# Kernel tuning notes

Hardware: AMD Instinct MI355X
Metric: run time of the kernel (lower is better)

## Reference

```python
import jax, jax.numpy as jnp
import numpy as np

B, L, D, K, V = 128, 50, 64, 1024, 100000


def setup_inputs() -> dict:
    key = jax.random.key(0)
    ks = jax.random.split(key, 10)
    s = 0.05
    return {
        "history_item_ids": jax.random.randint(ks[0], (B, L), 0, V, dtype=jnp.int32),
        "history_item_masks": jax.random.randint(ks[1], (B, L), 0, 2, dtype=jnp.int32),
        "embedding_table": jax.random.normal(ks[2], (V, D), jnp.float32) * s,
        "code_book": jax.random.normal(ks[3], (K, D), jnp.float32) * 0.1,
        "Wq": jax.random.normal(ks[4], (D, D), jnp.float32) * s,
        "bq": jnp.zeros((D,), jnp.float32),
        "Wk": jax.random.normal(ks[5], (D, D), jnp.float32) * s,
        "bk": jnp.zeros((D,), jnp.float32),
        "Wv": jax.random.normal(ks[6], (D, D), jnp.float32) * s,
        "bv": jnp.zeros((D,), jnp.float32),
        "W_enc": jax.random.normal(ks[7], (2 * D, D), jnp.float32) * s,
        "b_enc": jnp.zeros((D,), jnp.float32),
    }


def reference(history_item_ids, history_item_masks, embedding_table, code_book,
              Wq, bq, Wk, bk, Wv, bv, W_enc, b_enc):
    # mask out padded history positions
    mask = (history_item_masks >= 1).astype(jnp.float32)          # [B, L]
    h = embedding_table[history_item_ids] * mask[..., None]       # [B, L, D]

    # self_attn: attention over ALL B*L flattened tokens (cross-batch, as original)
    flat = h.reshape(-1, D)                                       # [B*L, D]
    q = flat @ Wq + bq
    k = flat @ Wk + bk
    v = flat @ Wv + bv
    scores = (q @ k.T) / jnp.sqrt(jnp.float32(D))                 # [B*L, B*L]
    h = (jax.nn.softmax(scores, axis=-1) @ v).reshape(B, L, D)

    denom = mask.sum(axis=1, keepdims=True)                       # [B, 1]
    hist_mean = h.sum(axis=1) / (denom + 1e-9)                    # [B, D]

    # get_quantized: pairwise sq distances + argmin + codebook lookup
    f = h.reshape(-1, D)                                          # [B*L, D]
    d2 = (jnp.sum(f * f, axis=1, keepdims=True)
          + jnp.sum(code_book * code_book, axis=1)
          - 2.0 * f @ code_book.T)                                # [B*L, K]
    idx = jnp.argmin(d2, axis=1)                                  # [B*L]
    vq = code_book[idx].reshape(B, L, D)                          # one_hot @ code_book == gather
    vq_mean = vq.sum(axis=1) / denom                              # [B, D]

    x = jnp.concatenate([vq_mean, hist_mean], axis=-1)            # [B, 2D]
    return x @ W_enc + b_enc                                      # [B, D]
```

## Files before the change

kernel.cpp:

```cpp
#include <hip/hip_runtime.h>

typedef __attribute__((ext_vector_type(8))) short bf16x8_t;
typedef __attribute__((ext_vector_type(4))) float f32x4_t;

#define B_   128
#define L_   50
#define D_   64
#define N_   6400
#define KC   1024
#define STRD 72

static __device__ __forceinline__ unsigned short f2b(float x) {
    union { float f; unsigned int u; } c; c.f = x;
    return (unsigned short)((c.u + 0x7FFFu + ((c.u >> 16) & 1u)) >> 16);
}

__global__ __launch_bounds__(256) void k_qkv(
    const int* __restrict__ ids, const int* __restrict__ masks,
    const float* __restrict__ emb,
    const float* __restrict__ Wq, const float* __restrict__ bq,
    const float* __restrict__ Wk, const float* __restrict__ bk,
    const float* __restrict__ Wv, const float* __restrict__ bv,
    const float* __restrict__ cbf,
    unsigned short* __restrict__ q, unsigned short* __restrict__ k,
    unsigned short* __restrict__ vt,
    float* __restrict__ cn, unsigned short* __restrict__ cbb,
    float4* __restrict__ zbase)
{
    const int tid = threadIdx.x;
    if (blockIdx.x >= 404) {
        const float4 z = make_float4(0.f, 0.f, 0.f, 0.f);
        for (int i = (blockIdx.x - 404) * 256 + tid; i < 108096; i += 26 * 256)
            zbase[i] = z;
        return;
    }
    if (blockIdx.x >= 400) {
        const int c = (blockIdx.x - 400) * 256 + tid;
        float s = 0.f;
        #pragma unroll
        for (int d4 = 0; d4 < 16; ++d4) {
            float4 x = ((const float4*)cbf)[c * 16 + d4];
            s = fmaf(x.x, x.x, s); s = fmaf(x.y, x.y, s);
            s = fmaf(x.z, x.z, s); s = fmaf(x.w, x.w, s);
            ushort4 u;
            u.x = f2b(x.x); u.y = f2b(x.y); u.z = f2b(x.z); u.w = f2b(x.w);
            *(ushort4*)&cbb[c * 64 + d4 * 4] = u;
        }
        cn[c] = s;
        return;
    }

    __shared__ float Ws[3 * 64 * 64];
    __shared__ float hs[16][64];
    const int n0  = blockIdx.x * 16;

    {
        const float4* wq4 = (const float4*)Wq;
        const float4* wk4 = (const float4*)Wk;
        const float4* wv4 = (const float4*)Wv;
        float4* ws4 = (float4*)Ws;
        #pragma unroll
        for (int i = 0; i < 4; ++i) ws4[i*256 + tid]        = wq4[i*256 + tid];
        #pragma unroll
        for (int i = 0; i < 4; ++i) ws4[1024 + i*256 + tid] = wk4[i*256 + tid];
        #pragma unroll
        for (int i = 0; i < 4; ++i) ws4[2048 + i*256 + tid] = wv4[i*256 + tid];
    }
    {
        const int t  = tid >> 4, c4 = tid & 15;
        const int n  = n0 + t;
        const int id = ids[n];
        const float m = (masks[n] >= 1) ? 1.0f : 0.0f;
        float4 e = ((const float4*)emb)[id * 16 + c4];
        ((float4*)&hs[t][0])[c4] = make_float4(e.x*m, e.y*m, e.z*m, e.w*m);
    }
    __syncthreads();

    const int j  = tid & 63;
    const int tg = tid >> 6;
    const float bqj = bq[j], bkj = bk[j], bvj = bv[j];
    #pragma unroll
    for (int p = 0; p < 4; ++p) {
        const int t = p * 4 + tg;
        float aq = bqj, ak = bkj, av = bvj;
        #pragma unroll 8
        for (int d = 0; d < 64; ++d) {
            const float hd = hs[t][d];
            aq = fmaf(hd, Ws[d*64 + j],        aq);
            ak = fmaf(hd, Ws[4096 + d*64 + j], ak);
            av = fmaf(hd, Ws[8192 + d*64 + j], av);
        }
        const int n = n0 + t;
        q[n*64 + j]   = f2b(aq);
        k[n*64 + j]   = f2b(ak);
        vt[j*N_ + n]  = f2b(av);
    }
}

__global__ __launch_bounds__(256, 4) void k_attn(
    const unsigned short* __restrict__ qg, const unsigned short* __restrict__ kg,
    const unsigned short* __restrict__ vtg,
    float* __restrict__ facc, float* __restrict__ lacc)
{
    __shared__ unsigned short Qs[32 * STRD];
    __shared__ unsigned short Ks[64 * STRD];
    __shared__ unsigned short Vts[64 * STRD];
    __shared__ unsigned short Ps[32 * STRD];
    __shared__ float Of[32 * 66];
    __shared__ float lred[2][32];

    const int tid  = threadIdx.x;
    const int qt   = blockIdx.x >> 2;
    const int sp   = blockIdx.x & 3;
    const int q0   = qt * 32;
    const int kvb  = sp * 1600;
    const int lane = tid & 63;
    const int w    = tid >> 6;
    const int m    = w & 1;
    const int s    = w >> 1;
    const int lr   = lane & 15;
    const int lg   = lane >> 4;

    {
        const int row = tid >> 3, ch = tid & 7;
        uint4 t = *(const uint4*)&qg[(q0 + row) * 64 + ch * 8];
        *(uint4*)&Qs[row * STRD + ch * 8] = t;
    }
    __syncthreads();
    const bf16x8_t qa0 = *(const bf16x8_t*)&Qs[(m*16 + lr) * STRD +  0 + lg*8];
    const bf16x8_t qa1 = *(const bf16x8_t*)&Qs[(m*16 + lr) * STRD + 32 + lg*8];

    f32x4_t o0 = {0.f,0.f,0.f,0.f}, o1 = {0.f,0.f,0.f,0.f};
    f32x4_t o2 = {0.f,0.f,0.f,0.f}, o3 = {0.f,0.f,0.f,0.f};
    float ls0 = 0.f, ls1 = 0.f, ls2 = 0.f, ls3 = 0.f;
    const float scale = 0.125f;

    for (int st = 0; st < 25; ++st) {
        __syncthreads();
        const int j0 = kvb + st * 64;
        {
            const int row = tid >> 3, ch = tid & 7;
            uint4 a = *(const uint4*)&kg [(j0 + row)      * 64 + ch*8];
            uint4 b = *(const uint4*)&kg [(j0 + row + 32) * 64 + ch*8];
            uint4 c = *(const uint4*)&vtg[ row       * N_ + j0 + ch*8];
            uint4 d = *(const uint4*)&vtg[(row + 32) * N_ + j0 + ch*8];
            *(uint4*)&Ks [ row      * STRD + ch*8] = a;
            *(uint4*)&Ks [(row+32)  * STRD + ch*8] = b;
            *(uint4*)&Vts[ row      * STRD + ch*8] = c;
            *(uint4*)&Vts[(row+32)  * STRD + ch*8] = d;
        }
        __syncthreads();

        #pragma unroll
        for (int t = 0; t < 2; ++t) {
            const int kcol = s*32 + t*16 + lr;
            bf16x8_t kb0 = *(const bf16x8_t*)&Ks[kcol * STRD +  0 + lg*8];
            bf16x8_t kb1 = *(const bf16x8_t*)&Ks[kcol * STRD + 32 + lg*8];
            f32x4_t acc = {0.f,0.f,0.f,0.f};
            acc = __builtin_amdgcn_mfma_f32_16x16x32_bf16(qa0, kb0, acc, 0, 0, 0);
            acc = __builtin_amdgcn_mfma_f32_16x16x32_bf16(qa1, kb1, acc, 0, 0, 0);
            const float p0 = __expf(acc[0] * scale);
            const float p1 = __expf(acc[1] * scale);
            const float p2 = __expf(acc[2] * scale);
            const float p3 = __expf(acc[3] * scale);
            ls0 += p0; ls1 += p1; ls2 += p2; ls3 += p3;
            const int rb = (m*16 + lg*4) * STRD + kcol;
            Ps[rb           ] = f2b(p0);
            Ps[rb +   STRD  ] = f2b(p1);
            Ps[rb + 2*STRD  ] = f2b(p2);
            Ps[rb + 3*STRD  ] = f2b(p3);
        }

        const bf16x8_t pa = *(const bf16x8_t*)&Ps[(m*16 + lr) * STRD + s*32 + lg*8];
        {
            bf16x8_t vb;
            vb = *(const bf16x8_t*)&Vts[( 0 + lr) * STRD + s*32 + lg*8];
            o0 = __builtin_amdgcn_mfma_f32_16x16x32_bf16(pa, vb, o0, 0, 0, 0);
            vb = *(const bf16x8_t*)&Vts[(16 + lr) * STRD + s*32 + lg*8];
            o1 = __builtin_amdgcn_mfma_f32_16x16x32_bf16(pa, vb, o1, 0, 0, 0);
            vb = *(const bf16x8_t*)&Vts[(32 + lr) * STRD + s*32 + lg*8];
            o2 = __builtin_amdgcn_mfma_f32_16x16x32_bf16(pa, vb, o2, 0, 0, 0);
            vb = *(const bf16x8_t*)&Vts[(48 + lr) * STRD + s*32 + lg*8];
            o3 = __builtin_amdgcn_mfma_f32_16x16x32_bf16(pa, vb, o3, 0, 0, 0);
        }
    }

    #pragma unroll
    for (int off = 1; off <= 8; off <<= 1) {
        ls0 += __shfl_xor(ls0, off);
        ls1 += __shfl_xor(ls1, off);
        ls2 += __shfl_xor(ls2, off);
        ls3 += __shfl_xor(ls3, off);
    }
    if (lr == 0) {
        const int rb = m*16 + lg*4;
        lred[s][rb    ] = ls0;
        lred[s][rb + 1] = ls1;
        lred[s][rb + 2] = ls2;
        lred[s][rb + 3] = ls3;
    }

    if (s == 0) {
        #pragma unroll
        for (int r = 0; r < 4; ++r) {
            const int row = m*16 + lg*4 + r;
            Of[row*66 +  0 + lr] = o0[r];
            Of[row*66 + 16 + lr] = o1[r];
            Of[row*66 + 32 + lr] = o2[r];
            Of[row*66 + 48 + lr] = o3[r];
        }
    }
    __syncthreads();
    if (s == 1) {
        #pragma unroll
        for (int r = 0; r < 4; ++r) {
            const int row = m*16 + lg*4 + r;
            float* dst = &facc[(q0 + row) * 64];
            atomicAdd(&dst[ 0 + lr], Of[row*66 +  0 + lr] + o0[r]);
            atomicAdd(&dst[16 + lr], Of[row*66 + 16 + lr] + o1[r]);
            atomicAdd(&dst[32 + lr], Of[row*66 + 32 + lr] + o2[r]);
            atomicAdd(&dst[48 + lr], Of[row*66 + 48 + lr] + o3[r]);
        }
    }
    if (tid < 32) atomicAdd(&lacc[q0 + tid], lred[0][tid] + lred[1][tid]);
}

__global__ __launch_bounds__(64) void k_argmin(
    const float* __restrict__ facc, const float* __restrict__ lacc,
    const unsigned short* __restrict__ cbb,
    const float* __restrict__ cn, const float* __restrict__ cbf,
    float* __restrict__ vqsum, float* __restrict__ hisum)
{
    __shared__ int   sidx[16];
    __shared__ float sinv[16];
    const int lane = threadIdx.x;
    const int n0   = blockIdx.x * 16;
    const int lr   = lane & 15, lg = lane >> 4;
    const int row  = n0 + lr;

    const float inv = 1.0f / lacc[row];
    if (lg == 0) sinv[lr] = inv;
    float4 a0 = *(const float4*)&facc[row*64 +      lg*8];
    float4 a1 = *(const float4*)&facc[row*64 +      lg*8 + 4];
    float4 a2 = *(const float4*)&facc[row*64 + 32 + lg*8];
    float4 a3 = *(const float4*)&facc[row*64 + 32 + lg*8 + 4];
    bf16x8_t fa0, fa1;
    fa0[0] = (short)f2b(a0.x*inv); fa0[1] = (short)f2b(a0.y*inv);
    fa0[2] = (short)f2b(a0.z*inv); fa0[3] = (short)f2b(a0.w*inv);
    fa0[4] = (short)f2b(a1.x*inv); fa0[5] = (short)f2b(a1.y*inv);
    fa0[6] = (short)f2b(a1.z*inv); fa0[7] = (short)f2b(a1.w*inv);
    fa1[0] = (short)f2b(a2.x*inv); fa1[1] = (short)f2b(a2.y*inv);
    fa1[2] = (short)f2b(a2.z*inv); fa1[3] = (short)f2b(a2.w*inv);
    fa1[4] = (short)f2b(a3.x*inv); fa1[5] = (short)f2b(a3.y*inv);
    fa1[6] = (short)f2b(a3.z*inv); fa1[7] = (short)f2b(a3.w*inv);

    float best0 = 3.0e38f, best1 = 3.0e38f, best2 = 3.0e38f, best3 = 3.0e38f;
    int   bi0 = 0, bi1 = 0, bi2 = 0, bi3 = 0;

    #pragma unroll 4
    for (int st = 0; st < 64; ++st) {
        const int crow = st * 16 + lr;
        bf16x8_t cb0 = *(const bf16x8_t*)&cbb[crow * 64 +  0 + lg*8];
        bf16x8_t cb1 = *(const bf16x8_t*)&cbb[crow * 64 + 32 + lg*8];
        const float cnv = cn[crow];
        f32x4_t acc = {0.f,0.f,0.f,0.f};
        acc = __builtin_amdgcn_mfma_f32_16x16x32_bf16(fa0, cb0, acc, 0, 0, 0);
        acc = __builtin_amdgcn_mfma_f32_16x16x32_bf16(fa1, cb1, acc, 0, 0, 0);
        const float d0 = fmaf(-2.f, acc[0], cnv);
        const float d1 = fmaf(-2.f, acc[1], cnv);
        const float d2 = fmaf(-2.f, acc[2], cnv);
        const float d3 = fmaf(-2.f, acc[3], cnv);
        if (d0 < best0) { best0 = d0; bi0 = crow; }
        if (d1 < best1) { best1 = d1; bi1 = crow; }
        if (d2 < best2) { best2 = d2; bi2 = crow; }
        if (d3 < best3) { best3 = d3; bi3 = crow; }
    }

    #pragma unroll
    for (int off = 1; off <= 8; off <<= 1) {
        float ov; int oi;
        ov = __shfl_xor(best0, off); oi = __shfl_xor(bi0, off);
        if (ov < best0 || (ov == best0 && oi < bi0)) { best0 = ov; bi0 = oi; }
        ov = __shfl_xor(best1, off); oi = __shfl_xor(bi1, off);
        if (ov < best1 || (ov == best1 && oi < bi1)) { best1 = ov; bi1 = oi; }
        ov = __shfl_xor(best2, off); oi = __shfl_xor(bi2, off);
        if (ov < best2 || (ov == best2 && oi < bi2)) { best2 = ov; bi2 = oi; }
        ov = __shfl_xor(best3, off); oi = __shfl_xor(bi3, off);
        if (ov < best3 || (ov == best3 && oi < bi3)) { best3 = ov; bi3 = oi; }
    }
    if (lr == 0) {
        sidx[lg*4 + 0] = bi0;
        sidx[lg*4 + 1] = bi1;
        sidx[lg*4 + 2] = bi2;
        sidx[lg*4 + 3] = bi3;
    }
    __syncthreads();

    const int d  = lane;
    const int b0 = n0 / 50;
    const int r0 = n0 - b0 * 50;
    float vq0 = 0.f, hi0 = 0.f, vq1 = 0.f, hi1 = 0.f;
    #pragma unroll
    for (int t = 0; t < 16; ++t) {
        const float hv = facc[(n0 + t) * 64 + d] * sinv[t];
        const float vv = cbf[sidx[t] * 64 + d];
        if (r0 + t < 50) { vq0 += vv; hi0 += hv; }
        else             { vq1 += vv; hi1 += hv; }
    }
    atomicAdd(&vqsum[b0*64 + d], vq0);
    atomicAdd(&hisum[b0*64 + d], hi0);
    if (r0 + 15 >= 50) {
        atomicAdd(&vqsum[(b0+1)*64 + d], vq1);
        atomicAdd(&hisum[(b0+1)*64 + d], hi1);
    }
}

__global__ __launch_bounds__(64) void k_final(
    const float* __restrict__ vqsum, const float* __restrict__ hisum,
    const int* __restrict__ masks,
    const float* __restrict__ Wenc, const float* __restrict__ benc,
    float* __restrict__ out)
{
    __shared__ float xs[128];
    const int b = blockIdx.x, d = threadIdx.x;
    float dn = 0.f;
    for (int l = 0; l < L_; ++l) dn += (masks[b*L_ + l] >= 1) ? 1.0f : 0.0f;
    xs[d]      = vqsum[b*64 + d] / dn;
    xs[64 + d] = hisum[b*64 + d] / (dn + 1e-9f);
    __syncthreads();
    float acc = benc[d];
    #pragma unroll 8
    for (int t = 0; t < 128; ++t) acc = fmaf(xs[t], Wenc[t*64 + d], acc);
    out[b*64 + d] = acc;
}

extern "C" void kernel_launch(void* const* d_in, const int* in_sizes, int n_in,
                              void* d_out, int out_size, void* d_ws, size_t ws_size,
                              hipStream_t stream)
{
    const int*   ids   = (const int*)  d_in[0];
    const int*   masks = (const int*)  d_in[1];
    const float* emb   = (const float*)d_in[2];
    const float* cb    = (const float*)d_in[3];
    const float* Wq    = (const float*)d_in[4];
    const float* bq    = (const float*)d_in[5];
    const float* Wk    = (const float*)d_in[6];
    const float* bk    = (const float*)d_in[7];
    const float* Wv    = (const float*)d_in[8];
    const float* bv    = (const float*)d_in[9];
    const float* Wenc  = (const float*)d_in[10];
    const float* benc  = (const float*)d_in[11];
    float* out = (float*)d_out;

    char* w = (char*)d_ws;
    unsigned short* qb    = (unsigned short*)(w);
    unsigned short* kb    = (unsigned short*)(w +  819200);
    unsigned short* vtb   = (unsigned short*)(w + 1638400);
    float*          facc  = (float*)        (w + 2457600);
    float*          lacc  = (float*)        (w + 4096000);
    float*          vqsum = (float*)        (w + 4121600);
    float*          hisum = (float*)        (w + 4154368);
    float*          cn    = (float*)        (w + 4187136);
    unsigned short* cbb   = (unsigned short*)(w + 4191232);
    float4*         zbase = (float4*)       (w + 2457600);

    hipLaunchKernelGGL(k_qkv,    dim3(430), dim3(256), 0, stream,
                       ids, masks, emb, Wq, bq, Wk, bk, Wv, bv, cb,
                       qb, kb, vtb, cn, cbb, zbase);
    hipLaunchKernelGGL(k_attn,   dim3(800), dim3(256), 0, stream,
                       qb, kb, vtb, facc, lacc);
    hipLaunchKernelGGL(k_argmin, dim3(400), dim3(64),  0, stream,
                       facc, lacc, cbb, cn, cb, vqsum, hisum);
    hipLaunchKernelGGL(k_final,  dim3(128), dim3(64),  0, stream,
                       vqsum, hisum, masks, Wenc, benc, out);
}
```

Before: 172.7 us.

## Replace attention atomics with per-split partials and fuse final projection into VQ kernel

The attention kernel now writes each KV-split's partial output and row-sum to separate buffers instead of atomically accumulating into a zeroed array. The argmin kernel sums the four partials itself. It also fuses the final encoder projection, counting mask entries with wave shuffles and accumulating linearly into out, which the QKV kernel pre-fills with the bias. This drops a kernel launch, the workspace zeroing and the contention on many float atomics. In exchange it writes and reads four times more partial data, and the output atomics make summation order nondeterministic.

```diff
diff --git a/kernel.cpp b/kernel.cpp
--- a/kernel.cpp
+++ b/kernel.cpp
@@ -21,17 +21,15 @@
     const float* __restrict__ Wq, const float* __restrict__ bq,
     const float* __restrict__ Wk, const float* __restrict__ bk,
     const float* __restrict__ Wv, const float* __restrict__ bv,
-    const float* __restrict__ cbf,
+    const float* __restrict__ cbf, const float* __restrict__ benc,
     unsigned short* __restrict__ q, unsigned short* __restrict__ k,
     unsigned short* __restrict__ vt,
     float* __restrict__ cn, unsigned short* __restrict__ cbb,
-    float4* __restrict__ zbase)
+    float* __restrict__ out)
 {
     const int tid = threadIdx.x;
     if (blockIdx.x >= 404) {
-        const float4 z = make_float4(0.f, 0.f, 0.f, 0.f);
-        for (int i = (blockIdx.x - 404) * 256 + tid; i < 108096; i += 26 * 256)
-            zbase[i] = z;
+        for (int i = tid; i < B_ * 64; i += 256) out[i] = benc[i & 63];
         return;
     }
     if (blockIdx.x >= 400) {
@@ -100,7 +98,7 @@
 __global__ __launch_bounds__(256, 4) void k_attn(
     const unsigned short* __restrict__ qg, const unsigned short* __restrict__ kg,
     const unsigned short* __restrict__ vtg,
-    float* __restrict__ facc, float* __restrict__ lacc)
+    float* __restrict__ opart, float* __restrict__ lpart)
 {
     __shared__ unsigned short Qs[32 * STRD];
     __shared__ unsigned short Ks[64 * STRD];
@@ -212,47 +210,56 @@
     }
     __syncthreads();
     if (s == 1) {
+        float* op = opart + ((size_t)sp * N_ + q0) * 64;
         #pragma unroll
         for (int r = 0; r < 4; ++r) {
             const int row = m*16 + lg*4 + r;
-            float* dst = &facc[(q0 + row) * 64];
-            atomicAdd(&dst[ 0 + lr], Of[row*66 +  0 + lr] + o0[r]);
-            atomicAdd(&dst[16 + lr], Of[row*66 + 16 + lr] + o1[r]);
-            atomicAdd(&dst[32 + lr], Of[row*66 + 32 + lr] + o2[r]);
-            atomicAdd(&dst[48 + lr], Of[row*66 + 48 + lr] + o3[r]);
-        }
-    }
-    if (tid < 32) atomicAdd(&lacc[q0 + tid], lred[0][tid] + lred[1][tid]);
-}
-
-__global__ __launch_bounds__(64) void k_argmin(
-    const float* __restrict__ facc, const float* __restrict__ lacc,
-    const unsigned short* __restrict__ cbb,
-    const float* __restrict__ cn, const float* __restrict__ cbf,
-    float* __restrict__ vqsum, float* __restrict__ hisum)
+            op[row*64 +  0 + lr] = Of[row*66 +  0 + lr] + o0[r];
+            op[row*64 + 16 + lr] = Of[row*66 + 16 + lr] + o1[r];
+            op[row*64 + 32 + lr] = Of[row*66 + 32 + lr] + o2[r];
+            op[row*64 + 48 + lr] = Of[row*66 + 48 + lr] + o3[r];
+        }
+    }
+    if (tid < 32) lpart[sp*N_ + q0 + tid] = lred[0][tid] + lred[1][tid];
+}
+
+__global__ __launch_bounds__(64) void k_vq(
+    const float* __restrict__ opart, const float* __restrict__ lpart,
+    const unsigned short* __restrict__ cbb, const float* __restrict__ cn,
+    const float* __restrict__ cbf, const int* __restrict__ masks,
+    const float* __restrict__ Wenc, float* __restrict__ out)
 {
-    __shared__ int   sidx[16];
-    __shared__ float sinv[16];
     const int lane = threadIdx.x;
     const int n0   = blockIdx.x * 16;
     const int lr   = lane & 15, lg = lane >> 4;
     const int row  = n0 + lr;
 
-    const float inv = 1.0f / lacc[row];
-    if (lg == 0) sinv[lr] = inv;
-    float4 a0 = *(const float4*)&facc[row*64 +      lg*8];
-    float4 a1 = *(const float4*)&facc[row*64 +      lg*8 + 4];
-    float4 a2 = *(const float4*)&facc[row*64 + 32 + lg*8];
-    float4 a3 = *(const float4*)&facc[row*64 + 32 + lg*8 + 4];
+    const float l = lpart[row] + lpart[N_ + row] + lpart[2*N_ + row] + lpart[3*N_ + row];
+    const float inv = 1.0f / l;
+
+    float fr[16];
+    #pragma unroll
+    for (int h = 0; h < 2; ++h) {
+        const int base = row*64 + h*32 + lg*8;
+        float4 s0 = *(const float4*)&opart[base];
+        float4 s1 = *(const float4*)&opart[(size_t)N_*64   + base];
+        float4 s2 = *(const float4*)&opart[(size_t)N_*64*2 + base];
+        float4 s3 = *(const float4*)&opart[(size_t)N_*64*3 + base];
+        float4 t0 = *(const float4*)&opart[base + 4];
+        float4 t1 = *(const float4*)&opart[(size_t)N_*64   + base + 4];
+        float4 t2 = *(const float4*)&opart[(size_t)N_*64*2 + base + 4];
+        float4 t3 = *(const float4*)&opart[(size_t)N_*64*3 + base + 4];
+        fr[h*8+0] = ((s0.x+s1.x)+s2.x)+s3.x;  fr[h*8+1] = ((s0.y+s1.y)+s2.y)+s3.y;
+        fr[h*8+2] = ((s0.z+s1.z)+s2.z)+s3.z;  fr[h*8+3] = ((s0.w+s1.w)+s2.w)+s3.w;
+        fr[h*8+4] = ((t0.x+t1.x)+t2.x)+t3.x;  fr[h*8+5] = ((t0.y+t1.y)+t2.y)+t3.y;
+        fr[h*8+6] = ((t0.z+t1.z)+t2.z)+t3.z;  fr[h*8+7] = ((t0.w+t1.w)+t2.w)+t3.w;
+    }
     bf16x8_t fa0, fa1;
-    fa0[0] = (short)f2b(a0.x*inv); fa0[1] = (short)f2b(a0.y*inv);
-    fa0[2] = (short)f2b(a0.z*inv); fa0[3] = (short)f2b(a0.w*inv);
-    fa0[4] = (short)f2b(a1.x*inv); fa0[5] = (short)f2b(a1.y*inv);
-    fa0[6] = (short)f2b(a1.z*inv); fa0[7] = (short)f2b(a1.w*inv);
-    fa1[0] = (short)f2b(a2.x*inv); fa1[1] = (short)f2b(a2.y*inv);
-    fa1[2] = (short)f2b(a2.z*inv); fa1[3] = (short)f2b(a2.w*inv);
-    fa1[4] = (short)f2b(a3.x*inv); fa1[5] = (short)f2b(a3.y*inv);
-    fa1[6] = (short)f2b(a3.z*inv); fa1[7] = (short)f2b(a3.w*inv);
+    #pragma unroll
+    for (int i = 0; i < 8; ++i) {
+        fa0[i] = (short)f2b(fr[i]     * inv);
+        fa1[i] = (short)f2b(fr[8 + i] * inv);
+    }
 
     float best0 = 3.0e38f, best1 = 3.0e38f, best2 = 3.0e38f, best3 = 3.0e38f;
     int   bi0 = 0, bi1 = 0, bi2 = 0, bi3 = 0;
@@ -288,13 +295,6 @@
         ov = __shfl_xor(best3, off); oi = __shfl_xor(bi3, off);
         if (ov < best3 || (ov == best3 && oi < bi3)) { best3 = ov; bi3 = oi; }
     }
-    if (lr == 0) {
-        sidx[lg*4 + 0] = bi0;
-        sidx[lg*4 + 1] = bi1;
-        sidx[lg*4 + 2] = bi2;
-        sidx[lg*4 + 3] = bi3;
-    }
-    __syncthreads();
 
     const int d  = lane;
     const int b0 = n0 / 50;
@@ -302,36 +302,52 @@
     float vq0 = 0.f, hi0 = 0.f, vq1 = 0.f, hi1 = 0.f;
     #pragma unroll
     for (int t = 0; t < 16; ++t) {
-        const float hv = facc[(n0 + t) * 64 + d] * sinv[t];
-        const float vv = cbf[sidx[t] * 64 + d];
+        int ci;
+        switch (t & 3) {
+            case 0:  ci = __shfl(bi0, (t >> 2) * 16); break;
+            case 1:  ci = __shfl(bi1, (t >> 2) * 16); break;
+            case 2:  ci = __shfl(bi2, (t >> 2) * 16); break;
+            default: ci = __shfl(bi3, (t >> 2) * 16); break;
+        }
+        const float invt = __shfl(inv, t);
+        const int   nb   = (n0 + t) * 64 + d;
+        const float hv = (((opart[nb] + opart[(size_t)N_*64 + nb])
+                         + opart[(size_t)N_*64*2 + nb]) + opart[(size_t)N_*64*3 + nb]) * invt;
+        const float vv = cbf[ci * 64 + d];
         if (r0 + t < 50) { vq0 += vv; hi0 += hv; }
         else             { vq1 += vv; hi1 += hv; }
     }
-    atomicAdd(&vqsum[b0*64 + d], vq0);
-    atomicAdd(&hisum[b0*64 + d], hi0);
+
+    int mv0 = (lane < 50) ? ((masks[b0*50 + lane] >= 1) ? 1 : 0) : 0;
+    #pragma unroll
+    for (int off = 1; off <= 32; off <<= 1) mv0 += __shfl_xor(mv0, off);
+    const float dn0 = (float)mv0;
+
+    {
+        const float iv = 1.0f / dn0, ih = 1.0f / (dn0 + 1e-9f);
+        float c0 = 0.f;
+        #pragma unroll 8
+        for (int dp = 0; dp < 64; ++dp) {
+            c0 = fmaf(__shfl(vq0, dp) * iv, Wenc[dp*64 + d], c0);
+            c0 = fmaf(__shfl(hi0, dp) * ih, Wenc[(64 + dp)*64 + d], c0);
+        }
+        atomicAdd(&out[b0*64 + d], c0);
+    }
     if (r0 + 15 >= 50) {
-        atomicAdd(&vqsum[(b0+1)*64 + d], vq1);
-        atomicAdd(&hisum[(b0+1)*64 + d], hi1);
-    }
-}
-
-__global__ __launch_bounds__(64) void k_final(
-    const float* __restrict__ vqsum, const float* __restrict__ hisum,
-    const int* __restrict__ masks,
-    const float* __restrict__ Wenc, const float* __restrict__ benc,
-    float* __restrict__ out)
-{
-    __shared__ float xs[128];
-    const int b = blockIdx.x, d = threadIdx.x;
-    float dn = 0.f;
-    for (int l = 0; l < L_; ++l) dn += (masks[b*L_ + l] >= 1) ? 1.0f : 0.0f;
-    xs[d]      = vqsum[b*64 + d] / dn;
-    xs[64 + d] = hisum[b*64 + d] / (dn + 1e-9f);
-    __syncthreads();
-    float acc = benc[d];
-    #pragma unroll 8
-    for (int t = 0; t < 128; ++t) acc = fmaf(xs[t], Wenc[t*64 + d], acc);
-    out[b*64 + d] = acc;
+        const int b1 = b0 + 1;
+        int mv1 = (lane < 50) ? ((masks[b1*50 + lane] >= 1) ? 1 : 0) : 0;
+        #pragma unroll
+        for (int off = 1; off <= 32; off <<= 1) mv1 += __shfl_xor(mv1, off);
+        const float dn1 = (float)mv1;
+        const float iv = 1.0f / dn1, ih = 1.0f / (dn1 + 1e-9f);
+        float c1 = 0.f;
+        #pragma unroll 8
+        for (int dp = 0; dp < 64; ++dp) {
+            c1 = fmaf(__shfl(vq1, dp) * iv, Wenc[dp*64 + d], c1);
+            c1 = fmaf(__shfl(hi1, dp) * ih, Wenc[(64 + dp)*64 + d], c1);
+        }
+        atomicAdd(&out[b1*64 + d], c1);
+    }
 }
 
 extern "C" void kernel_launch(void* const* d_in, const int* in_sizes, int n_in,
@@ -356,21 +372,16 @@
     unsigned short* qb    = (unsigned short*)(w);
     unsigned short* kb    = (unsigned short*)(w +  819200);
     unsigned short* vtb   = (unsigned short*)(w + 1638400);
-    float*          facc  = (float*)        (w + 2457600);
-    float*          lacc  = (float*)        (w + 4096000);
-    float*          vqsum = (float*)        (w + 4121600);
-    float*          hisum = (float*)        (w + 4154368);
-    float*          cn    = (float*)        (w + 4187136);
-    unsigned short* cbb   = (unsigned short*)(w + 4191232);
-    float4*         zbase = (float4*)       (w + 2457600);
-
-    hipLaunchKernelGGL(k_qkv,    dim3(430), dim3(256), 0, stream,
-                       ids, masks, emb, Wq, bq, Wk, bk, Wv, bv, cb,
-                       qb, kb, vtb, cn, cbb, zbase);
-    hipLaunchKernelGGL(k_attn,   dim3(800), dim3(256), 0, stream,
-                       qb, kb, vtb, facc, lacc);
-    hipLaunchKernelGGL(k_argmin, dim3(400), dim3(64),  0, stream,
-                       facc, lacc, cbb, cn, cb, vqsum, hisum);
-    hipLaunchKernelGGL(k_final,  dim3(128), dim3(64),  0, stream,
-                       vqsum, hisum, masks, Wenc, benc, out);
-}
+    float*          opart = (float*)        (w + 2457600);
+    float*          lpart = (float*)        (w + 9011200);
+    float*          cn    = (float*)        (w + 9113600);
+    unsigned short* cbb   = (unsigned short*)(w + 9117696);
+
+    hipLaunchKernelGGL(k_qkv,  dim3(405), dim3(256), 0, stream,
+                       ids, masks, emb, Wq, bq, Wk, bk, Wv, bv, cb, benc,
+                       qb, kb, vtb, cn, cbb, out);
+    hipLaunchKernelGGL(k_attn, dim3(800), dim3(256), 0, stream,
+                       qb, kb, vtb, opart, lpart);
+    hipLaunchKernelGGL(k_vq,   dim3(400), dim3(64),  0, stream,
+                       opart, lpart, cbb, cn, cb, masks, Wenc, out);
+}
```

Measured after the change: 157.7 us. -8.7%, faster.
